# Kernel optimization log

Hardware: AMD Instinct MI355X
Metric: run time of the kernel (lower is better)

Reference implementation:

```python
import jax, jax.numpy as jnp
import numpy as np

B, T, D, U = 64, 512, 1024, 1024


def hard_sigmoid(x):
    # keras hard_sigmoid: clip(0.2*x + 0.5, 0, 1)
    return jnp.clip(0.2 * x + 0.5, 0.0, 1.0)


def setup_inputs() -> dict:
    key = jax.random.key(0)
    ks = jax.random.split(key, 6)
    x = jax.random.normal(ks[0], (B, T, D), jnp.float32)
    # glorot-ish scaled params
    kernel = jax.random.normal(ks[1], (D, 4 * U), jnp.float32) * (1.0 / np.sqrt(D).astype(np.float32))
    recurrent_kernel = jax.random.normal(ks[2], (U, 4 * U), jnp.float32) * (1.0 / np.sqrt(U).astype(np.float32))
    peephole_kernel = jax.random.normal(ks[3], (U, 3 * U), jnp.float32) * (1.0 / np.sqrt(U).astype(np.float32))
    projection_kernel = jax.random.normal(ks[4], (U, U), jnp.float32) * (1.0 / np.sqrt(U).astype(np.float32))
    # unit_forget_bias: [zeros(U), ones(U), zeros(2U)] for (i, f, c, o)
    bias = jnp.concatenate([jnp.zeros((U,), jnp.float32), jnp.ones((U,), jnp.float32), jnp.zeros((2 * U,), jnp.float32)])
    h0 = jnp.zeros((B, U), jnp.float32)
    c0 = jnp.zeros((B, U), jnp.float32)
    return {"x": x, "h0": h0, "c0": c0, "kernel": kernel, "recurrent_kernel": recurrent_kernel,
            "peephole_kernel": peephole_kernel, "projection_kernel": projection_kernel, "bias": bias}


def reference(x, h0, c0, kernel, recurrent_kernel, peephole_kernel, projection_kernel, bias):
    U_ = h0.shape[-1]
    Pi = peephole_kernel[:, :U_]
    Pf = peephole_kernel[:, U_:2 * U_]
    Po = peephole_kernel[:, 2 * U_:3 * U_]

    def step(carry, x_t):
        h, c = carry
        # fused gate pre-activations: [B, 4U]
        z = x_t @ kernel + h @ recurrent_kernel + bias
        zi, zf, zc, zo = jnp.split(z, 4, axis=-1)
        i = hard_sigmoid(zi + c @ Pi)            # input gate w/ peephole on c_{t-1}
        f = hard_sigmoid(zf + c @ Pf)            # forget gate w/ peephole on c_{t-1}
        c_new = f * c + i * jnp.tanh(zc)
        o = hard_sigmoid(zo + c_new @ Po)        # output gate w/ peephole on c_t
        # residual LSTM: project tanh(c_t), add residual input, gate by o
        h_new = o * (jnp.tanh(c_new) @ projection_kernel + x_t)
        return (h_new, c_new), h_new

    xs = jnp.swapaxes(x, 0, 1)  # [T, B, D]
    (_, _), hs = jax.lax.scan(step, (h0, c0), xs)
    return jnp.swapaxes(hs, 0, 1)  # [B, T, U]
```

## Files before the change

### kernel.cpp

```cpp
#include <hip/hip_runtime.h>
#include <cstdint>
#include <cstddef>

#define NB 64
#define NT 512
#define ND 1024
#define NU 1024

typedef short s16x8 __attribute__((ext_vector_type(8)));
typedef float f32x4 __attribute__((ext_vector_type(4)));
typedef unsigned int u32x2 __attribute__((ext_vector_type(2)));
typedef unsigned int u32x4 __attribute__((ext_vector_type(4)));
typedef unsigned short u16;

__device__ __forceinline__ u16 f2bf(float f) {
  unsigned int u = __float_as_uint(f);
  u += 0x7fffu + ((u >> 16) & 1u);
  return (u16)(u >> 16);
}
__device__ __forceinline__ float bf2f(u16 s) {
  return __uint_as_float(((unsigned int)s) << 16);
}
__device__ __forceinline__ float hsig(float x) {
  return fminf(fmaxf(0.2f * x + 0.5f, 0.0f), 1.0f);
}
__device__ __forceinline__ float ftanh(float x) {
  float e = __expf(2.0f * x);
  return 1.0f - 2.0f / (e + 1.0f);
}
__device__ __forceinline__ f32x4 mfma16(s16x8 a, s16x8 b, f32x4 c) {
  return __builtin_amdgcn_mfma_f32_16x16x32_bf16(a, b, c, 0, 0, 0);
}

__device__ __forceinline__ void atomic_swap_u32(unsigned int* p, unsigned int v) {
  asm volatile("global_atomic_swap %0, %1, off" :: "v"(p), "v"(v) : "memory");
}
__device__ __forceinline__ void atomic_swap_u64(unsigned int* p, u32x2 v) {
  asm volatile("global_atomic_swap_x2 %0, %1, off" :: "v"(p), "v"(v) : "memory");
}

template <int STAGED>
__device__ __forceinline__ void ldx4(s16x8& d, const u16* a) {
  if constexpr (STAGED)
    asm volatile("global_load_dwordx4 %0, %1, off" : "=v"(d) : "v"(a));
  else
    asm volatile("global_load_dwordx4 %0, %1, off sc0 sc1" : "=v"(d) : "v"(a));
}

#define WAIT_VM0() do { \
    asm volatile("s_waitcnt vmcnt(0)" ::: "memory"); \
    __builtin_amdgcn_sched_barrier(0); \
  } while (0)
#define WAIT_VM(N) do { \
    asm volatile("s_waitcnt vmcnt(" #N ")" ::: "memory"); \
    __builtin_amdgcn_sched_barrier(0); \
  } while (0)

__global__ __launch_bounds__(256) void wt_cvt(const float* __restrict__ W,
                                              u16* __restrict__ Wt) {
  __shared__ u16 T[64][65];
  const int tid = threadIdx.x;
  const int k0 = (blockIdx.x & 15) * 64;
  const int n0 = (blockIdx.x >> 4) * 64;
  const int r = tid >> 2, c4 = (tid & 3) * 16;
  {
    const float* src = W + (size_t)(k0 + r) * 4096 + n0 + c4;
#pragma unroll
    for (int j = 0; j < 4; ++j) {
      float4 v = ((const float4*)src)[j];
      T[r][c4 + j * 4 + 0] = f2bf(v.x); T[r][c4 + j * 4 + 1] = f2bf(v.y);
      T[r][c4 + j * 4 + 2] = f2bf(v.z); T[r][c4 + j * 4 + 3] = f2bf(v.w);
    }
  }
  __syncthreads();
  {
    u16 tmp[16];
#pragma unroll
    for (int i = 0; i < 16; ++i) tmp[i] = T[c4 + i][r];
    u16* dst = Wt + (size_t)(n0 + r) * 1024 + k0 + c4;
    *(s16x8*)dst = *(s16x8*)tmp;
    *(s16x8*)(dst + 8) = *(s16x8*)(tmp + 8);
  }
}

template <int WT>
__global__ __launch_bounds__(256) void xw_gemm(const float* __restrict__ X,
                                               const float* __restrict__ W,
                                               const u16* __restrict__ Wt,
                                               u16* __restrict__ XW) {
  __shared__ u16 Al[128][72];
  __shared__ u16 Bl[128][72];
  const int tid = threadIdx.x;
  const int lane = tid & 63;
  const int wv = tid >> 6;
  const int m0 = (blockIdx.x >> 5) * 128;
  const int n0 = (blockIdx.x & 31) * 128;
  f32x4 acc[4][4];
#pragma unroll
  for (int i = 0; i < 4; ++i)
#pragma unroll
    for (int j = 0; j < 4; ++j) acc[i][j] = (f32x4){0.f, 0.f, 0.f, 0.f};

  for (int kt = 0; kt < 1024; kt += 64) {
    {
      const int r = tid >> 1, hh = (tid & 1) * 32;
      const float* src = X + (size_t)(m0 + r) * 1024 + kt + hh;
      u16* dst = &Al[r][hh];
      if constexpr (WT) {
#pragma unroll
        for (int j = 0; j < 4; ++j) {
          float4 v0 = ((const float4*)src)[2 * j];
          float4 v1 = ((const float4*)src)[2 * j + 1];
          u32x4 q;
          q[0] = ((unsigned)f2bf(v0.y) << 16) | f2bf(v0.x);
          q[1] = ((unsigned)f2bf(v0.w) << 16) | f2bf(v0.z);
          q[2] = ((unsigned)f2bf(v1.y) << 16) | f2bf(v1.x);
          q[3] = ((unsigned)f2bf(v1.w) << 16) | f2bf(v1.z);
          *(u32x4*)(dst + j * 8) = q;
        }
      } else {
#pragma unroll
        for (int j = 0; j < 8; ++j) {
          float4 v = ((const float4*)src)[j];
          dst[j * 4 + 0] = f2bf(v.x); dst[j * 4 + 1] = f2bf(v.y);
          dst[j * 4 + 2] = f2bf(v.z); dst[j * 4 + 3] = f2bf(v.w);
        }
      }
    }
    if constexpr (WT) {
      const int n = tid >> 1, kh = (tid & 1) * 32;
      const u16* src = Wt + (size_t)(n0 + n) * 1024 + kt + kh;
      u16* dst = &Bl[n][kh];
#pragma unroll
      for (int j = 0; j < 4; ++j)
        *(s16x8*)(dst + j * 8) = *(const s16x8*)(src + j * 8);
    } else {
      const int kr = tid >> 2, q = (tid & 3) * 32;
      const float* src = W + (size_t)(kt + kr) * 4096 + n0 + q;
#pragma unroll
      for (int j = 0; j < 8; ++j) {
        float4 v = ((const float4*)src)[j];
        const int n = q + j * 4;
        Bl[n + 0][kr] = f2bf(v.x); Bl[n + 1][kr] = f2bf(v.y);
        Bl[n + 2][kr] = f2bf(v.z); Bl[n + 3][kr] = f2bf(v.w);
      }
    }
    __syncthreads();
    const int wm = (wv >> 1) * 64, wn = (wv & 1) * 64;
    const int row = lane & 15, kq = (lane >> 4) * 8;
#pragma unroll
    for (int ks = 0; ks < 2; ++ks) {
      s16x8 af[4], bq[4];
#pragma unroll
      for (int i = 0; i < 4; ++i) af[i] = *(const s16x8*)&Al[wm + i * 16 + row][ks * 32 + kq];
#pragma unroll
      for (int j = 0; j < 4; ++j) bq[j] = *(const s16x8*)&Bl[wn + j * 16 + row][ks * 32 + kq];
#pragma unroll
      for (int i = 0; i < 4; ++i)
#pragma unroll
        for (int j = 0; j < 4; ++j) acc[i][j] = mfma16(af[i], bq[j], acc[i][j]);
    }
    __syncthreads();
  }
  const int wm = (wv >> 1) * 64, wn = (wv & 1) * 64;
  const int col16 = lane & 15, rq = (lane >> 4) * 4;
#pragma unroll
  for (int i = 0; i < 4; ++i)
#pragma unroll
    for (int j = 0; j < 4; ++j)
#pragma unroll
      for (int q = 0; q < 4; ++q) {
        const int m = m0 + wm + i * 16 + rq + q;
        const int n = n0 + wn + j * 16 + col16;
        const int t = m & 511, b = m >> 9;
        const int g = n >> 10, uu = n & 1023;
        const int ugrp = uu >> 3, ul2 = uu & 7;
        XW[(((size_t)ugrp * 512 + t) * 64 + b) * 32 + ul2 * 4 + g] = f2bf(acc[i][j][q]);
      }
}

__global__ void init_comm(const float* __restrict__ h0, const float* __restrict__ c0,
                          u16* hini, u16* cini) {
  const int i = blockIdx.x * 256 + threadIdx.x;
  hini[i] = f2bf(h0[i]);
  cini[i] = f2bf(c0[i]);
}

__device__ __forceinline__ void gbar_arrive(unsigned int* flags, int bid, int tid,
                                            unsigned int ep) {
  __syncthreads();
  if (tid == 0) atomic_swap_u32(flags + bid * 16, ep);
}
__device__ __forceinline__ void gbar_poll(unsigned int* flags, int bid, int tid,
                                          unsigned int ep, int stagger) {
  unsigned int* f = flags + ((((tid & 127) << 1) | (bid & 1)) * 16);
  if (stagger && (tid & 128)) __builtin_amdgcn_s_sleep(7);
  for (;;) {
    unsigned int v;
    asm volatile("global_load_dword %0, %1, off sc0 sc1\n\ts_waitcnt vmcnt(0)"
                 : "=v"(v) : "v"(f) : "memory");
    if (v >= ep) break;
    __builtin_amdgcn_s_sleep(1);
  }
}

#define WLDS_B   (64 * 1032 * 2)
#define SCR_S    44
#define ZOFF     WLDS_B
#define POFF     (ZOFF + 32 * SCR_S * 4)
#define OOFF     (POFF + 32 * SCR_S * 4)
#define SMEM_B   (OOFF + 32 * SCR_S * 4)
#define STEP_E   65536

template <int STAGED>
__global__ __launch_bounds__(256, 1) void lstm_loop(
    const float* __restrict__ rec, const float* __restrict__ peep,
    const float* __restrict__ projw, const float* __restrict__ bias,
    const float* __restrict__ x, const u16* __restrict__ xw,
    float* __restrict__ out,
    u16* hini, u16* cini, u16* thsg,
    u16* hst, u16* cst, u16* thst,
    unsigned int* flags, const float* __restrict__ c0) {
  extern __shared__ char smem[];
  u16 (*wlds)[1032] = (u16(*)[1032])smem;
  float (*zlds)[SCR_S] = (float(*)[SCR_S])(smem + ZOFF);
  float (*plds)[SCR_S] = (float(*)[SCR_S])(smem + POFF);
  float (*olds)[SCR_S] = (float(*)[SCR_S])(smem + OOFF);

  const int tid = threadIdx.x;
  const int lane = tid & 63;
  const int wv = tid >> 6;
  const int bid = blockIdx.x;
  const int ugrp = bid >> 1;
  const int row0 = (bid & 1) * 32;
  const int u0 = ugrp * 8;

  for (int g = 0; g < 8; ++g) {
    const int c = g * 8 + (tid & 3) * 2;
    const float* sp; int stride, scol;
    if (c < 32)      { sp = rec;   stride = 4096; scol = (c >> 3) * 1024 + u0 + (c & 7); }
    else if (c < 48) { sp = peep;  stride = 3072; scol = ((c - 32) >> 3) * 1024 + u0 + (c & 7); }
    else if (c < 56) { sp = peep;  stride = 3072; scol = 2048 + u0 + (c & 7); }
    else             { sp = projw; stride = 1024; scol = u0 + (c - 56); }
#pragma unroll 4
    for (int p = 0; p < 16; ++p) {
      const int k = p * 64 + (tid >> 2);
      float2 v = *(const float2*)(sp + (size_t)k * stride + scol);
      wlds[c][k] = f2bf(v.x);
      wlds[c + 1][k] = f2bf(v.y);
    }
  }

  const int r = tid >> 3;
  const int ul = tid & 7;
  const int brow = row0 + r;
  const int u = u0 + ul;
  const float b_i = bias[u], b_f = bias[1024 + u], b_c = bias[2048 + u], b_o = bias[3072 + u];
  float cstv = c0[brow * 1024 + u];

  const int fcol = lane & 15;
  const int kofs = (lane >> 4) * 8;

  s16x8 av[32];
  u32x2 xwp;
  float xp;

  {
    const u16* xr0 = xw + (((size_t)ugrp * 512 + 0) * 64 + brow) * 32 + ul * 4;
    asm volatile("global_load_dwordx2 %0, %1, off" : "=v"(xwp) : "v"(xr0));
    const float* xs0 = x + (size_t)brow * (512 * 1024) + u;
    asm volatile("global_load_dword %0, %1, off" : "=v"(xp) : "v"(xs0));
  }
  if (wv < 2) {
    const u16* ap = cini + (size_t)(row0 + wv * 16 + fcol) * 1024 + kofs;
#pragma unroll
    for (int kt = 0; kt < 32; ++kt)
      asm volatile("global_load_dwordx4 %0, %1, off sc0 sc1"
                   : "=v"(av[kt]) : "v"(ap + kt * 32));
  }
  WAIT_VM0();
  __syncthreads();

  for (int t = 0; t < NT; ++t) {
    float zo_reg, xres, hv;
    const size_t xo = (size_t)brow * (512 * 1024) + (size_t)t * 1024 + u;

    const u16* hsrc; u16* cpub; u16* thpub; const u16* csrc; const u16* thsrc; u16* hpub;
    if constexpr (STAGED) {
      hsrc  = t ? (hst + (size_t)(t - 1) * STEP_E) : hini;
      hpub  = hst + (size_t)t * STEP_E;
      cpub  = cst + (size_t)t * STEP_E;   csrc  = cpub;
      thpub = thst + (size_t)t * STEP_E;  thsrc = thpub;
    } else {
      hsrc = hini; hpub = hini; cpub = cini; csrc = cini; thpub = thsg; thsrc = thsg;
    }

    if (wv >= 2) {
      gbar_poll(flags, bid, tid, 2 * (unsigned)t, 0);
      const int rt = wv - 2;
      const u16* ap = hsrc + (size_t)(row0 + rt * 16 + fcol) * 1024 + kofs;
#pragma unroll
      for (int kt = 0; kt < 32; ++kt) ldx4<STAGED>(av[kt], ap + kt * 32);
      WAIT_VM0();
      f32x4 accA = {0.f, 0.f, 0.f, 0.f}, accB = {0.f, 0.f, 0.f, 0.f};
      const u16* bp0 = &wlds[fcol][kofs];
      const u16* bp1 = &wlds[16 + fcol][kofs];
#pragma unroll
      for (int kt = 0; kt < 32; ++kt) {
        accA = mfma16(av[kt], *(const s16x8*)(bp0 + kt * 32), accA);
        accB = mfma16(av[kt], *(const s16x8*)(bp1 + kt * 32), accB);
      }
      const int srow = rt * 16 + (lane >> 4) * 4;
#pragma unroll
      for (int q = 0; q < 4; ++q) {
        zlds[srow + q][fcol] = accA[q];
        zlds[srow + q][16 + fcol] = accB[q];
      }
    } else {
      f32x4 accP = {0.f, 0.f, 0.f, 0.f};
      const u16* bp = &wlds[32 + fcol][kofs];
#pragma unroll
      for (int kt = 0; kt < 32; ++kt)
        accP = mfma16(av[kt], *(const s16x8*)(bp + kt * 32), accP);
      const int srow = wv * 16 + (lane >> 4) * 4;
#pragma unroll
      for (int q = 0; q < 4; ++q) plds[srow + q][fcol] = accP[q];
      WAIT_VM(1);
    }
    __syncthreads();
    {
      const float xw_i = bf2f((u16)(xwp[0] & 0xffffu));
      const float xw_f = bf2f((u16)(xwp[0] >> 16));
      const float xw_c = bf2f((u16)(xwp[1] & 0xffffu));
      const float xw_o = bf2f((u16)(xwp[1] >> 16));
      xres = xp;
      const float zi = zlds[r][ul]      + xw_i + b_i + plds[r][ul];
      const float zf = zlds[r][8 + ul]  + xw_f + b_f + plds[r][8 + ul];
      const float zc = zlds[r][16 + ul] + xw_c + b_c;
      zo_reg         = zlds[r][24 + ul] + xw_o + b_o;
      const float ig = hsig(zi), fg = hsig(zf);
      cstv = fg * cstv + ig * ftanh(zc);
      const float th = ftanh(cstv);
      const unsigned int cb = f2bf(cstv), tb = f2bf(th);
      const unsigned int cp = ((unsigned)__shfl_xor((int)cb, 1) << 16) | cb;
      const unsigned int tp = ((unsigned)__shfl_xor((int)tb, 1) << 16) | tb;
      const unsigned int cp2 = (unsigned)__shfl_xor((int)cp, 2);
      const unsigned int tp2 = (unsigned)__shfl_xor((int)tp, 2);
      if ((ul & 3) == 0) {
        u32x2 cq; cq[0] = cp; cq[1] = cp2;
        u32x2 tq; tq[0] = tp; tq[1] = tp2;
        atomic_swap_u64((unsigned int*)(cpub + brow * 1024 + u), cq);
        atomic_swap_u64((unsigned int*)(thpub + brow * 1024 + u), tq);
      }
    }
    WAIT_VM0();
    gbar_arrive(flags, bid, tid, 2 * t + 1);
    gbar_poll(flags, bid, tid, 2 * t + 1, 1);
    __syncthreads();

    {
      const int prt = wv & 1;
      const u16* ap = ((wv < 2) ? csrc : thsrc)
                      + (size_t)(row0 + prt * 16 + fcol) * 1024 + kofs;
#pragma unroll
      for (int kt = 0; kt < 32; ++kt) ldx4<STAGED>(av[kt], ap + kt * 32);
      WAIT_VM0();
      f32x4 acc = {0.f, 0.f, 0.f, 0.f};
      const u16* bp = &wlds[48 + fcol][kofs];
#pragma unroll
      for (int kt = 0; kt < 32; ++kt)
        acc = mfma16(av[kt], *(const s16x8*)(bp + kt * 32), acc);
      const int srow = prt * 16 + (lane >> 4) * 4;
      if (wv < 2) {
        if (fcol < 8) {
#pragma unroll
          for (int q = 0; q < 4; ++q) olds[srow + q][fcol] = acc[q];
        }
      } else {
        if (fcol >= 8) {
#pragma unroll
          for (int q = 0; q < 4; ++q) olds[srow + q][fcol] = acc[q];
        }
      }
    }
    __syncthreads();
    {
      const float og = hsig(zo_reg + olds[r][ul]);
      const float pv = olds[r][8 + ul] + xres;
      hv = og * pv;
      const unsigned int hb = f2bf(hv);
      const unsigned int hp = ((unsigned)__shfl_xor((int)hb, 1) << 16) | hb;
      const unsigned int hp2 = (unsigned)__shfl_xor((int)hp, 2);
      if ((ul & 3) == 0) {
        u32x2 hq; hq[0] = hp; hq[1] = hp2;
        atomic_swap_u64((unsigned int*)(hpub + brow * 1024 + u), hq);
      }
      const int tn = (t + 1 < NT) ? (t + 1) : t;
      const u16* xrn = xw + (((size_t)ugrp * 512 + tn) * 64 + brow) * 32 + ul * 4;
      asm volatile("global_load_dwordx2 %0, %1, off" : "=v"(xwp) : "v"(xrn));
      const float* xsn = x + (size_t)brow * (512 * 1024) + (size_t)tn * 1024 + u;
      asm volatile("global_load_dword %0, %1, off" : "=v"(xp) : "v"(xsn));
      asm volatile("global_store_dword %0, %1, off" :: "v"(out + xo), "v"(hv) : "memory");
      WAIT_VM(3);
    }
    gbar_arrive(flags, bid, tid, 2 * t + 2);
  }
}

extern "C" void kernel_launch(void* const* d_in, const int* in_sizes, int n_in,
                              void* d_out, int out_size, void* d_ws, size_t ws_size,
                              hipStream_t stream) {
  const float* x    = (const float*)d_in[0];
  const float* h0   = (const float*)d_in[1];
  const float* c0   = (const float*)d_in[2];
  const float* W    = (const float*)d_in[3];
  const float* R    = (const float*)d_in[4];
  const float* P    = (const float*)d_in[5];
  const float* PRJ  = (const float*)d_in[6];
  const float* bias = (const float*)d_in[7];
  float* out = (float*)d_out;
  char* ws = (char*)d_ws;

  const size_t XW_BYTES = (size_t)32768 * 4096 * 2;
  size_t off = XW_BYTES;
  u16* xw   = (u16*)ws;
  u16* hini = (u16*)(ws + off); off += 131072;
  u16* cini = (u16*)(ws + off); off += 131072;
  u16* thsg = (u16*)(ws + off); off += 131072;
  unsigned int* flags = (unsigned int*)(ws + off); off += 16384;
  const size_t base_need = off;
  u16* hst = (u16*)(ws + off); off += (size_t)NT * 131072;
  u16* cst = (u16*)(ws + off); off += (size_t)NT * 131072;
  u16* thst = (u16*)(ws + off); off += (size_t)NT * 131072;
  const size_t staged_need = off;
  u16* Wt = (u16*)(ws + off); off += (size_t)4096 * 1024 * 2;
  const size_t wt_need = off;
  if (ws_size < base_need) return;
  const int staged = (ws_size >= staged_need) ? 1 : 0;
  const int wt = (ws_size >= wt_need) ? 1 : 0;

  (void)hipFuncSetAttribute(reinterpret_cast<const void*>(&lstm_loop<1>),
                            hipFuncAttributeMaxDynamicSharedMemorySize, 160 * 1024);
  (void)hipFuncSetAttribute(reinterpret_cast<const void*>(&lstm_loop<0>),
                            hipFuncAttributeMaxDynamicSharedMemorySize, 160 * 1024);

  hipMemsetAsync(flags, 0, 16384, stream);
  hipLaunchKernelGGL(init_comm, dim3(256), dim3(256), 0, stream, h0, c0, hini, cini);
  if (wt) {
    hipLaunchKernelGGL(wt_cvt, dim3(1024), dim3(256), 0, stream, W, Wt);
    hipLaunchKernelGGL((xw_gemm<1>), dim3(8192), dim3(256), 0, stream, x, W, Wt, xw);
  } else {
    hipLaunchKernelGGL((xw_gemm<0>), dim3(8192), dim3(256), 0, stream, x, W, Wt, xw);
  }

  void* args[15];
  args[0] = (void*)&R;     args[1] = (void*)&P;     args[2] = (void*)&PRJ;
  args[3] = (void*)&bias;  args[4] = (void*)&x;     args[5] = (void*)&xw;
  args[6] = (void*)&out;   args[7] = (void*)&hini;  args[8] = (void*)&cini;
  args[9] = (void*)&thsg;  args[10] = (void*)&hst;  args[11] = (void*)&cst;
  args[12] = (void*)&thst; args[13] = (void*)&flags; args[14] = (void*)&c0;

  const void* fn = staged ? (const void*)&lstm_loop<1> : (const void*)&lstm_loop<0>;
  hipError_t e = hipLaunchCooperativeKernel(fn, dim3(256), dim3(256),
                                            args, (unsigned int)SMEM_B, stream);
  if (e != hipSuccess) {
    if (staged)
      hipLaunchKernelGGL((lstm_loop<1>), dim3(256), dim3(256), SMEM_B, stream,
                         R, P, PRJ, bias, x, xw, out, hini, cini, thsg,
                         hst, cst, thst, flags, c0);
    else
      hipLaunchKernelGGL((lstm_loop<0>), dim3(256), dim3(256), SMEM_B, stream,
                         R, P, PRJ, bias, x, xw, out, hini, cini, thsg,
                         hst, cst, thst, flags, c0);
  }
}
```

Measured before the change: 6.958 ms.

## Repartition LSTM blocks to 16 units x 16 rows with register-resident recurrent weights

```diff
diff --git a/kernel.cpp b/kernel.cpp
--- a/kernel.cpp
+++ b/kernel.cpp
@@ -174,8 +174,8 @@
         const int n = n0 + wn + j * 16 + col16;
         const int t = m & 511, b = m >> 9;
         const int g = n >> 10, uu = n & 1023;
-        const int ugrp = uu >> 3, ul2 = uu & 7;
-        XW[(((size_t)ugrp * 512 + t) * 64 + b) * 32 + ul2 * 4 + g] = f2bf(acc[i][j][q]);
+        const int ugrp = uu >> 4, ul2 = uu & 15;
+        XW[(((size_t)ugrp * 512 + t) * 64 + b) * 64 + ul2 * 4 + g] = f2bf(acc[i][j][q]);
       }
 }
 
@@ -191,10 +191,9 @@
   __syncthreads();
   if (tid == 0) atomic_swap_u32(flags + bid * 16, ep);
 }
-__device__ __forceinline__ void gbar_poll(unsigned int* flags, int bid, int tid,
-                                          unsigned int ep, int stagger) {
-  unsigned int* f = flags + ((((tid & 127) << 1) | (bid & 1)) * 16);
-  if (stagger && (tid & 128)) __builtin_amdgcn_s_sleep(7);
+__device__ __forceinline__ void gbar_poll(unsigned int* flags, int rq, int tid,
+                                          unsigned int ep) {
+  unsigned int* f = flags + ((((tid & 63) << 2) | rq) * 16);
   for (;;) {
     unsigned int v;
     asm volatile("global_load_dword %0, %1, off sc0 sc1\n\ts_waitcnt vmcnt(0)"
@@ -202,14 +201,14 @@
     if (v >= ep) break;
     __builtin_amdgcn_s_sleep(1);
   }
+  __builtin_amdgcn_sched_barrier(0);
 }
 
 #define WLDS_B   (64 * 1032 * 2)
-#define SCR_S    44
 #define ZOFF     WLDS_B
-#define POFF     (ZOFF + 32 * SCR_S * 4)
-#define OOFF     (POFF + 32 * SCR_S * 4)
-#define SMEM_B   (OOFF + 32 * SCR_S * 4)
+#define POFF     (ZOFF + 16 * 68 * 4)
+#define OOFF     (POFF + 16 * 36 * 4)
+#define SMEM_B   (OOFF + 16 * 36 * 4)
 #define STEP_E   65536
 
 template <int STAGED>
@@ -218,30 +217,48 @@
     const float* __restrict__ projw, const float* __restrict__ bias,
     const float* __restrict__ x, const u16* __restrict__ xw,
     float* __restrict__ out,
-    u16* hini, u16* cini, u16* thsg,
+    u16* hini, u16* cini, u16* cb0, u16* cb1, u16* thsg,
     u16* hst, u16* cst, u16* thst,
     unsigned int* flags, const float* __restrict__ c0) {
   extern __shared__ char smem[];
   u16 (*wlds)[1032] = (u16(*)[1032])smem;
-  float (*zlds)[SCR_S] = (float(*)[SCR_S])(smem + ZOFF);
-  float (*plds)[SCR_S] = (float(*)[SCR_S])(smem + POFF);
-  float (*olds)[SCR_S] = (float(*)[SCR_S])(smem + OOFF);
+  float (*zlds)[68] = (float(*)[68])(smem + ZOFF);
+  float (*plds)[36] = (float(*)[36])(smem + POFF);
+  float (*olds)[36] = (float(*)[36])(smem + OOFF);
 
   const int tid = threadIdx.x;
   const int lane = tid & 63;
   const int wv = tid >> 6;
   const int bid = blockIdx.x;
-  const int ugrp = bid >> 1;
-  const int row0 = (bid & 1) * 32;
-  const int u0 = ugrp * 8;
-
+  const int ugrp = bid >> 2;
+  const int rq = bid & 3;
+  const int row0 = rq * 16;
+  const int u0 = ugrp * 16;
+  const int fcol = lane & 15;
+  const int kofs = (lane >> 4) * 8;
+
+  for (int g = 0; g < 8; ++g) {
+    const int c = g * 8 + (tid & 3) * 2;
+    const int scol = (c >> 4) * 1024 + u0 + (c & 15);
+#pragma unroll 4
+    for (int p = 0; p < 16; ++p) {
+      const int k = p * 64 + (tid >> 2);
+      float2 v = *(const float2*)(rec + (size_t)k * 4096 + scol);
+      wlds[c][k] = f2bf(v.x);
+      wlds[c + 1][k] = f2bf(v.y);
+    }
+  }
+  __syncthreads();
+  s16x8 breg[32];
+#pragma unroll
+  for (int kt = 0; kt < 32; ++kt)
+    breg[kt] = *(const s16x8*)&wlds[wv * 16 + fcol][kt * 32 + kofs];
+  __syncthreads();
   for (int g = 0; g < 8; ++g) {
     const int c = g * 8 + (tid & 3) * 2;
     const float* sp; int stride, scol;
-    if (c < 32)      { sp = rec;   stride = 4096; scol = (c >> 3) * 1024 + u0 + (c & 7); }
-    else if (c < 48) { sp = peep;  stride = 3072; scol = ((c - 32) >> 3) * 1024 + u0 + (c & 7); }
-    else if (c < 56) { sp = peep;  stride = 3072; scol = 2048 + u0 + (c & 7); }
-    else             { sp = projw; stride = 1024; scol = u0 + (c - 56); }
+    if (c < 48) { sp = peep;  stride = 3072; scol = (c >> 4) * 1024 + u0 + (c & 15); }
+    else        { sp = projw; stride = 1024; scol = u0 + (c & 15); }
 #pragma unroll 4
     for (int p = 0; p < 16; ++p) {
       const int k = p * 64 + (tid >> 2);
@@ -251,81 +268,84 @@
     }
   }
 
-  const int r = tid >> 3;
-  const int ul = tid & 7;
+  const int r = tid >> 4;
+  const int ul = tid & 15;
   const int brow = row0 + r;
   const int u = u0 + ul;
   const float b_i = bias[u], b_f = bias[1024 + u], b_c = bias[2048 + u], b_o = bias[3072 + u];
   float cstv = c0[brow * 1024 + u];
 
-  const int fcol = lane & 15;
-  const int kofs = (lane >> 4) * 8;
-
-  s16x8 av[32];
   u32x2 xwp;
   float xp;
-
   {
-    const u16* xr0 = xw + (((size_t)ugrp * 512 + 0) * 64 + brow) * 32 + ul * 4;
+    const u16* xr0 = xw + (((size_t)ugrp * 512 + 0) * 64 + brow) * 64 + ul * 4;
     asm volatile("global_load_dwordx2 %0, %1, off" : "=v"(xwp) : "v"(xr0));
     const float* xs0 = x + (size_t)brow * (512 * 1024) + u;
     asm volatile("global_load_dword %0, %1, off" : "=v"(xp) : "v"(xs0));
   }
-  if (wv < 2) {
-    const u16* ap = cini + (size_t)(row0 + wv * 16 + fcol) * 1024 + kofs;
-#pragma unroll
-    for (int kt = 0; kt < 32; ++kt)
-      asm volatile("global_load_dwordx4 %0, %1, off sc0 sc1"
-                   : "=v"(av[kt]) : "v"(ap + kt * 32));
-  }
-  WAIT_VM0();
   __syncthreads();
 
   for (int t = 0; t < NT; ++t) {
+    const size_t xo = (size_t)brow * (512 * 1024) + (size_t)t * 1024 + u;
     float zo_reg, xres, hv;
-    const size_t xo = (size_t)brow * (512 * 1024) + (size_t)t * 1024 + u;
-
-    const u16* hsrc; u16* cpub; u16* thpub; const u16* csrc; const u16* thsrc; u16* hpub;
+
+    const u16 *hsrc, *cpsrc, *csrc, *thsrc; u16 *cpub, *thpub, *hpub;
     if constexpr (STAGED) {
       hsrc  = t ? (hst + (size_t)(t - 1) * STEP_E) : hini;
+      cpsrc = t ? (cst + (size_t)(t - 1) * STEP_E) : cini;
+      cpub  = cst + (size_t)t * STEP_E;   csrc = cpub;
+      thpub = thst + (size_t)t * STEP_E;  thsrc = thpub;
       hpub  = hst + (size_t)t * STEP_E;
-      cpub  = cst + (size_t)t * STEP_E;   csrc  = cpub;
-      thpub = thst + (size_t)t * STEP_E;  thsrc = thpub;
     } else {
-      hsrc = hini; hpub = hini; cpub = cini; csrc = cini; thpub = thsg; thsrc = thsg;
-    }
-
-    if (wv >= 2) {
-      gbar_poll(flags, bid, tid, 2 * (unsigned)t, 0);
-      const int rt = wv - 2;
-      const u16* ap = hsrc + (size_t)(row0 + rt * 16 + fcol) * 1024 + kofs;
-#pragma unroll
-      for (int kt = 0; kt < 32; ++kt) ldx4<STAGED>(av[kt], ap + kt * 32);
+      hsrc = hini; hpub = hini;
+      cpub = (t & 1) ? cb1 : cb0; csrc = cpub;
+      cpsrc = (t == 0) ? cini : ((t & 1) ? cb0 : cb1);
+      thpub = thsg; thsrc = thsg;
+    }
+
+    s16x8 av[32];
+    if (wv < 2) {
+      s16x8 cv[32];
+      {
+        const u16* ap = cpsrc + (size_t)(row0 + fcol) * 1024 + kofs;
+#pragma unroll
+        for (int kt = 0; kt < 32; ++kt) ldx4<STAGED>(cv[kt], ap + kt * 32);
+      }
+      gbar_poll(flags, rq, tid, 2 * (unsigned)t);
+      f32x4 accP = {0.f, 0.f, 0.f, 0.f};
+      const u16* bp = &wlds[wv * 16 + fcol][kofs];
+#pragma unroll
+      for (int kt = 0; kt < 32; ++kt)
+        accP = mfma16(cv[kt], *(const s16x8*)(bp + kt * 32), accP);
+      {
+        const u16* ap = hsrc + (size_t)(row0 + fcol) * 1024 + kofs;
+#pragma unroll
+        for (int kt = 0; kt < 32; ++kt) ldx4<STAGED>(av[kt], ap + kt * 32);
+      }
       WAIT_VM0();
-      f32x4 accA = {0.f, 0.f, 0.f, 0.f}, accB = {0.f, 0.f, 0.f, 0.f};
-      const u16* bp0 = &wlds[fcol][kofs];
-      const u16* bp1 = &wlds[16 + fcol][kofs];
-#pragma unroll
-      for (int kt = 0; kt < 32; ++kt) {
-        accA = mfma16(av[kt], *(const s16x8*)(bp0 + kt * 32), accA);
-        accB = mfma16(av[kt], *(const s16x8*)(bp1 + kt * 32), accB);
-      }
-      const int srow = rt * 16 + (lane >> 4) * 4;
+      f32x4 accZ = {0.f, 0.f, 0.f, 0.f};
+#pragma unroll
+      for (int kt = 0; kt < 32; ++kt) accZ = mfma16(av[kt], breg[kt], accZ);
+      const int srow = (lane >> 4) * 4;
 #pragma unroll
       for (int q = 0; q < 4; ++q) {
-        zlds[srow + q][fcol] = accA[q];
-        zlds[srow + q][16 + fcol] = accB[q];
+        zlds[srow + q][wv * 16 + fcol] = accZ[q];
+        plds[srow + q][wv * 16 + fcol] = accP[q];
       }
     } else {
-      f32x4 accP = {0.f, 0.f, 0.f, 0.f};
-      const u16* bp = &wlds[32 + fcol][kofs];
-#pragma unroll
-      for (int kt = 0; kt < 32; ++kt)
-        accP = mfma16(av[kt], *(const s16x8*)(bp + kt * 32), accP);
-      const int srow = wv * 16 + (lane >> 4) * 4;
-#pragma unroll
-      for (int q = 0; q < 4; ++q) plds[srow + q][fcol] = accP[q];
-      WAIT_VM(1);
+      gbar_poll(flags, rq, tid, 2 * (unsigned)t);
+      {
+        const u16* ap = hsrc + (size_t)(row0 + fcol) * 1024 + kofs;
+#pragma unroll
+        for (int kt = 0; kt < 32; ++kt) ldx4<STAGED>(av[kt], ap + kt * 32);
+      }
+      WAIT_VM0();
+      f32x4 accZ = {0.f, 0.f, 0.f, 0.f};
+#pragma unroll
+      for (int kt = 0; kt < 32; ++kt) accZ = mfma16(av[kt], breg[kt], accZ);
+      const int srow = (lane >> 4) * 4;
+#pragma unroll
+      for (int q = 0; q < 4; ++q) zlds[srow + q][wv * 16 + fcol] = accZ[q];
     }
     __syncthreads();
     {
@@ -335,9 +355,9 @@
       const float xw_o = bf2f((u16)(xwp[1] >> 16));
       xres = xp;
       const float zi = zlds[r][ul]      + xw_i + b_i + plds[r][ul];
-      const float zf = zlds[r][8 + ul]  + xw_f + b_f + plds[r][8 + ul];
-      const float zc = zlds[r][16 + ul] + xw_c + b_c;
-      zo_reg         = zlds[r][24 + ul] + xw_o + b_o;
+      const float zf = zlds[r][16 + ul] + xw_f + b_f + plds[r][16 + ul];
+      const float zc = zlds[r][32 + ul] + xw_c + b_c;
+      zo_reg         = zlds[r][48 + ul] + xw_o + b_o;
       const float ig = hsig(zi), fg = hsig(zf);
       cstv = fg * cstv + ig * ftanh(zc);
       const float th = ftanh(cstv);
@@ -355,38 +375,27 @@
     }
     WAIT_VM0();
     gbar_arrive(flags, bid, tid, 2 * t + 1);
-    gbar_poll(flags, bid, tid, 2 * t + 1, 1);
-    __syncthreads();
-
-    {
-      const int prt = wv & 1;
-      const u16* ap = ((wv < 2) ? csrc : thsrc)
-                      + (size_t)(row0 + prt * 16 + fcol) * 1024 + kofs;
+
+    if (!STAGED || wv >= 2) gbar_poll(flags, rq, tid, 2 * t + 1);
+    if (wv >= 2) {
+      const u16* ap = ((wv == 2) ? csrc : thsrc)
+                      + (size_t)(row0 + fcol) * 1024 + kofs;
 #pragma unroll
       for (int kt = 0; kt < 32; ++kt) ldx4<STAGED>(av[kt], ap + kt * 32);
       WAIT_VM0();
       f32x4 acc = {0.f, 0.f, 0.f, 0.f};
-      const u16* bp = &wlds[48 + fcol][kofs];
+      const u16* bp = &wlds[wv * 16 + fcol][kofs];
 #pragma unroll
       for (int kt = 0; kt < 32; ++kt)
         acc = mfma16(av[kt], *(const s16x8*)(bp + kt * 32), acc);
-      const int srow = prt * 16 + (lane >> 4) * 4;
-      if (wv < 2) {
-        if (fcol < 8) {
-#pragma unroll
-          for (int q = 0; q < 4; ++q) olds[srow + q][fcol] = acc[q];
-        }
-      } else {
-        if (fcol >= 8) {
-#pragma unroll
-          for (int q = 0; q < 4; ++q) olds[srow + q][fcol] = acc[q];
-        }
-      }
+      const int srow = (lane >> 4) * 4;
+#pragma unroll
+      for (int q = 0; q < 4; ++q) olds[srow + q][(wv - 2) * 16 + fcol] = acc[q];
     }
     __syncthreads();
     {
       const float og = hsig(zo_reg + olds[r][ul]);
-      const float pv = olds[r][8 + ul] + xres;
+      const float pv = olds[r][16 + ul] + xres;
       hv = og * pv;
       const unsigned int hb = f2bf(hv);
       const unsigned int hp = ((unsigned)__shfl_xor((int)hb, 1) << 16) | hb;
@@ -396,7 +405,7 @@
         atomic_swap_u64((unsigned int*)(hpub + brow * 1024 + u), hq);
       }
       const int tn = (t + 1 < NT) ? (t + 1) : t;
-      const u16* xrn = xw + (((size_t)ugrp * 512 + tn) * 64 + brow) * 32 + ul * 4;
+      const u16* xrn = xw + (((size_t)ugrp * 512 + tn) * 64 + brow) * 64 + ul * 4;
       asm volatile("global_load_dwordx2 %0, %1, off" : "=v"(xwp) : "v"(xrn));
       const float* xsn = x + (size_t)brow * (512 * 1024) + (size_t)tn * 1024 + u;
       asm volatile("global_load_dword %0, %1, off" : "=v"(xp) : "v"(xsn));
@@ -426,11 +435,13 @@
   u16* xw   = (u16*)ws;
   u16* hini = (u16*)(ws + off); off += 131072;
   u16* cini = (u16*)(ws + off); off += 131072;
+  u16* cb0  = (u16*)(ws + off); off += 131072;
+  u16* cb1  = (u16*)(ws + off); off += 131072;
   u16* thsg = (u16*)(ws + off); off += 131072;
   unsigned int* flags = (unsigned int*)(ws + off); off += 16384;
   const size_t base_need = off;
-  u16* hst = (u16*)(ws + off); off += (size_t)NT * 131072;
-  u16* cst = (u16*)(ws + off); off += (size_t)NT * 131072;
+  u16* hst = (u16*)(ws + off);  off += (size_t)NT * 131072;
+  u16* cst = (u16*)(ws + off);  off += (size_t)NT * 131072;
   u16* thst = (u16*)(ws + off); off += (size_t)NT * 131072;
   const size_t staged_need = off;
   u16* Wt = (u16*)(ws + off); off += (size_t)4096 * 1024 * 2;
@@ -453,12 +464,13 @@
     hipLaunchKernelGGL((xw_gemm<0>), dim3(8192), dim3(256), 0, stream, x, W, Wt, xw);
   }
 
-  void* args[15];
+  void* args[17];
   args[0] = (void*)&R;     args[1] = (void*)&P;     args[2] = (void*)&PRJ;
   args[3] = (void*)&bias;  args[4] = (void*)&x;     args[5] = (void*)&xw;
   args[6] = (void*)&out;   args[7] = (void*)&hini;  args[8] = (void*)&cini;
-  args[9] = (void*)&thsg;  args[10] = (void*)&hst;  args[11] = (void*)&cst;
-  args[12] = (void*)&thst; args[13] = (void*)&flags; args[14] = (void*)&c0;
+  args[9] = (void*)&cb0;   args[10] = (void*)&cb1;  args[11] = (void*)&thsg;
+  args[12] = (void*)&hst;  args[13] = (void*)&cst;  args[14] = (void*)&thst;
+  args[15] = (void*)&flags; args[16] = (void*)&c0;
 
   const void* fn = staged ? (const void*)&lstm_loop<1> : (const void*)&lstm_loop<0>;
   hipError_t e = hipLaunchCooperativeKernel(fn, dim3(256), dim3(256),
@@ -466,11 +478,11 @@
   if (e != hipSuccess) {
     if (staged)
       hipLaunchKernelGGL((lstm_loop<1>), dim3(256), dim3(256), SMEM_B, stream,
-                         R, P, PRJ, bias, x, xw, out, hini, cini, thsg,
+                         R, P, PRJ, bias, x, xw, out, hini, cini, cb0, cb1, thsg,
                          hst, cst, thst, flags, c0);
     else
       hipLaunchKernelGGL((lstm_loop<0>), dim3(256), dim3(256), SMEM_B, stream,
-                         R, P, PRJ, bias, x, xw, out, hini, cini, thsg,
+                         R, P, PRJ, bias, x, xw, out, hini, cini, cb0, cb1, thsg,
                          hst, cst, thst, flags, c0);
   }
 }
```

Result: slower. 7.169 ms (+3.0%).
